# Kernel optimization log

Hardware: AMD Instinct MI355X
Metric: run time of the kernel (lower is better)

Reference implementation:

```python
import jax, jax.numpy as jnp
import numpy as np

B, F, N_SP, VIS_DIM, DIM, HEADS = 2, 16, 784, 512, 512, 8


def setup_inputs() -> dict:
    key = jax.random.key(0)
    k0, k1, k2 = jax.random.split(key, 3)
    x = jax.random.normal(k0, (B, F * N_SP, VIS_DIM), dtype=jnp.float32)
    # QKV: nn.Linear(vis_dim, dim*3, bias=False) -> weight [3*dim, vis_dim]
    Wqkv = jax.random.normal(k1, (3 * DIM, VIS_DIM), dtype=jnp.float32) * 0.02
    # proj: nn.Linear(dim, vis_dim) -> weight [vis_dim, dim], bias [vis_dim]
    Wproj = jax.random.normal(k2, (VIS_DIM, DIM), dtype=jnp.float32) * 0.02
    bproj = jnp.zeros((VIS_DIM,), dtype=jnp.float32)
    return {"x": x, "Wqkv": Wqkv, "Wproj": Wproj, "bproj": bproj,
            "spatial": N_SP, "f": F, "n": N_SP}


def reference(x, Wqkv, Wproj, bproj, spatial, f, n):
    # Factorized (divided space-time) SPATIAL attention:
    # einops_from='b (f n) d', einops_to='(b f) n d' -- attention over n within each frame.
    h = HEADS
    b, seq, _ = x.shape  # seq = f * n
    dim = Wqkv.shape[0] // 3
    hd = dim // h
    scale = hd ** -0.5

    qkv = x @ Wqkv.T                             # [b, f*n, 3*dim]
    q, k, v = jnp.split(qkv, 3, axis=-1)
    rs = lambda t: t.reshape(b, f, n, h, hd)     # b (f n) (h d) -> b f n h d
    q = rs(q) * scale
    k = rs(k)
    v = rs(v)

    # scores over spatial tokens within each (batch, frame, head)
    attn = jax.nn.softmax(jnp.einsum('bfihd,bfjhd->bfhij', q, k), axis=-1)
    out = jnp.einsum('bfhij,bfjhd->bfihd', attn, v)   # [b, f, n, h, hd]
    out = out.reshape(b, seq, dim)               # merge heads + restore (f n)
    return out @ Wproj.T + bproj                 # [b, f*n, vis_dim]
```

## Files before the change

kernel.cpp:

```cpp
#include <hip/hip_runtime.h>
#include <hip/hip_bf16.h>
#include <stdint.h>

using bf16 = __hip_bfloat16;
typedef __bf16 bf16x8 __attribute__((ext_vector_type(8)));
typedef float f32x4  __attribute__((ext_vector_type(4)));
typedef float f32x16 __attribute__((ext_vector_type(16)));

#define NB 2
#define NF 16
#define NSP 784
#define SEQ 12544
#define MROWS 25088
#define QSCALE 0.18033688011112042f

__device__ inline void gload16(const void* g, void* l) {
    __builtin_amdgcn_global_load_lds(
        (const __attribute__((address_space(1))) unsigned int*)g,
        (__attribute__((address_space(3))) unsigned int*)l, 16, 0, 0);
}
__device__ inline ushort f2bu(float x) {
    union { bf16 b; ushort u; } c; c.b = __float2bfloat16(x); return c.u;
}

__global__ __launch_bounds__(256)
void cvt_x_kernel(const float* __restrict__ x, ushort* __restrict__ xb, int n4) {
    int i = blockIdx.x * 256 + threadIdx.x;
    int stride = gridDim.x * 256;
    for (; i < n4; i += stride) {
        float4 v = ((const float4*)x)[i];
        ushort4 u;
        u.x = f2bu(v.x); u.y = f2bu(v.y); u.z = f2bu(v.z); u.w = f2bu(v.w);
        ((ushort4*)xb)[i] = u;
    }
}

__global__ __launch_bounds__(256)
void cvt_w_kernel(const float* __restrict__ wqkv, const float* __restrict__ wproj,
                  ushort* __restrict__ wqkvb, ushort* __restrict__ wpb) {
    int i = blockIdx.x * 256 + threadIdx.x;
    float4 v;
    ushort4 u;
    if (i < 196608) {
        float s = (i < 65536) ? QSCALE : 1.0f;
        v = ((const float4*)wqkv)[i];
        u.x = f2bu(v.x * s); u.y = f2bu(v.y * s);
        u.z = f2bu(v.z * s); u.w = f2bu(v.w * s);
        ((ushort4*)wqkvb)[i] = u;
    } else {
        int j = i - 196608;
        v = ((const float4*)wproj)[j];
        u.x = f2bu(v.x); u.y = f2bu(v.y); u.z = f2bu(v.z); u.w = f2bu(v.w);
        ((ushort4*)wpb)[j] = u;
    }
}

template<int EPI>
__global__ __launch_bounds__(256)
void gemm_mfma(const ushort* __restrict__ A, const ushort* __restrict__ W,
               const float* __restrict__ bias, ushort* __restrict__ outb,
               float* __restrict__ outf, int K, int ldc, int npan)
{
    constexpr int BK  = 64;
    constexpr int SWZ = 7;
    __shared__ ushort smem[16384];

    const int tid = threadIdx.x;
    const int bid = blockIdx.x;
    const int gsz = 4 * npan;
    const int r   = bid % gsz;
    const int m0 = ((bid / gsz) * 4 + (r & 3)) * 128;
    const int n0 = (r >> 2) * 128;
    const int l  = tid & 63;
    const int wv = tid >> 6;
    const int wm = wv >> 1, wn = wv & 1;
    const int lm = l & 15;
    const int koffb = (l >> 4) * 16;
    const int swz = (lm & SWZ) << 4;

    const int rsub = tid >> 3;
    const int cb0  = (tid & 7) * 16;
    const int wofs = (tid >> 6) * 512;

    const size_t ldb = (size_t)K * 2;
    const char* Ab = (const char*)A + (size_t)m0 * ldb;
    const char* Wb = (const char*)W + (size_t)n0 * ldb;

    f32x4 acc[4][4] = {};

    for (int k0 = 0; k0 < K; k0 += BK) {
        if (k0) __syncthreads();
#pragma unroll
        for (int i = 0; i < 4; ++i) {
            int row = i * 32 + rsub;
            int cbs = cb0 ^ ((row & SWZ) << 4);
            size_t roff = (size_t)row * ldb + (size_t)(k0 * 2 + cbs);
            gload16(Ab + roff, smem +        i * 2048 + wofs);
            gload16(Wb + roff, smem + 8192 + i * 2048 + wofs);
        }
        __syncthreads();

#pragma unroll
        for (int ks = 0; ks < 2; ++ks) {
            bf16x8 af[4], wf[4];
            const int cb = ((ks * 64 + koffb) ^ swz) >> 1;
#pragma unroll
            for (int f = 0; f < 4; ++f) {
                int rA = wm * 64 + f * 16 + lm;
                int rW = wn * 64 + f * 16 + lm;
                af[f] = *(const bf16x8*)&smem[rA * BK + cb];
                wf[f] = *(const bf16x8*)&smem[8192 + rW * BK + cb];
            }
            __builtin_amdgcn_s_setprio(1);
#pragma unroll
            for (int fm = 0; fm < 4; ++fm)
#pragma unroll
                for (int fn = 0; fn < 4; ++fn)
                    acc[fm][fn] = __builtin_amdgcn_mfma_f32_16x16x32_bf16(
                        wf[fn], af[fm], acc[fm][fn], 0, 0, 0);
            __builtin_amdgcn_s_setprio(0);
        }
    }

    const int ln4 = (l >> 4) * 4;
    if (EPI == 0) {
#pragma unroll
        for (int fm = 0; fm < 4; ++fm) {
            int m = m0 + wm * 64 + fm * 16 + lm;
            ushort* rowp = outb + (size_t)m * ldc + n0 + wn * 64 + ln4;
#pragma unroll
            for (int fn = 0; fn < 4; ++fn) {
                ushort4 u;
                u.x = f2bu(acc[fm][fn][0]); u.y = f2bu(acc[fm][fn][1]);
                u.z = f2bu(acc[fm][fn][2]); u.w = f2bu(acc[fm][fn][3]);
                *(ushort4*)(rowp + fn * 16) = u;
            }
        }
    } else {
#pragma unroll
        for (int fm = 0; fm < 4; ++fm) {
            int m = m0 + wm * 64 + fm * 16 + lm;
            float* rowp = outf + (size_t)m * ldc + n0 + wn * 64 + ln4;
#pragma unroll
            for (int fn = 0; fn < 4; ++fn) {
                float4 b4 = *(const float4*)&bias[n0 + wn * 64 + fn * 16 + ln4];
                float4 o;
                o.x = acc[fm][fn][0] + b4.x; o.y = acc[fm][fn][1] + b4.y;
                o.z = acc[fm][fn][2] + b4.z; o.w = acc[fm][fn][3] + b4.w;
                *(float4*)(rowp + fn * 16) = o;
            }
        }
    }
}

__global__ __launch_bounds__(256)
void vtrans(const ushort* __restrict__ qkv, ushort* __restrict__ vt)
{
    __shared__ __align__(16) ushort T[256][72];
    const int tid = threadIdx.x;
    const int pr  = blockIdx.x;
    const int c   = blockIdx.y;
    const int hh  = pr & 7, bfi = pr >> 3;
    const ushort* vsrc = qkv + (size_t)bfi * NSP * 1536 + 1024 + hh * 64;
    ushort* dst = vt + (size_t)pr * (64 * NSP);
    const int d = tid & 63, q = tid >> 6;

    const int j0 = c * 256;
    const int nj = (NSP - j0) < 256 ? (NSP - j0) : 256;
    if (tid < nj) {
        const ushort* src = vsrc + (size_t)(j0 + tid) * 1536;
#pragma unroll
        for (int u = 0; u < 8; ++u)
            *(uint4*)&T[tid][u * 8] = *(const uint4*)(src + u * 8);
    }
    __syncthreads();
    if (q * 64 < nj) {
        int cnt = nj - q * 64; if (cnt > 64) cnt = 64;
        union { uint4 u[8]; ushort s[64]; } buf;
#pragma unroll
        for (int jj = 0; jj < 64; ++jj)
            buf.s[jj] = T[q * 64 + jj][d];
        ushort* o = dst + (size_t)d * NSP + j0 + q * 64;
        if (cnt == 64) {
#pragma unroll
            for (int u = 0; u < 8; ++u) *(uint4*)(o + u * 8) = buf.u[u];
        } else {
#pragma unroll
            for (int u = 0; u < 2; ++u) *(uint4*)(o + u * 8) = buf.u[u];
        }
    }
}

__global__ __launch_bounds__(256, 4)
void attn_mfma(const ushort* __restrict__ qkv, const ushort* __restrict__ vt,
               ushort* __restrict__ oh)
{
    __shared__ __align__(16) ushort Ks[2][4096];
    __shared__ __align__(16) ushort Vs[2][4096];
    const int tid = threadIdx.x;
    const int l   = tid & 63;
    const int li  = l & 31;
    const int h5  = l >> 5;
    const int w   = tid >> 6;

    const int bid  = blockIdx.x;
    const int xcd  = bid & 7;
    const int slot = bid >> 3;
    const int pr   = (xcd << 5) + slot / 7;
    const int qt   = slot % 7;
    const int hh   = pr & 7;
    const int bfi  = pr >> 3;
    const size_t rowbase = (size_t)bfi * NSP;
    const int iq = qt * 128 + w * 32 + li;
    const bool qvalid = iq < NSP;
    const int iqc = qvalid ? iq : NSP - 1;

    bf16x8 qf[4];
    {
        const ushort* qrow = qkv + (rowbase + iqc) * 1536 + hh * 64 + h5 * 8;
#pragma unroll
        for (int ks = 0; ks < 4; ++ks)
            qf[ks] = *(const bf16x8*)(qrow + ks * 16);
    }

    const char* kb0   = (const char*)(qkv + rowbase * 1536 + 512 + hh * 64);
    const char* vbase = (const char*)(vt + (size_t)pr * (64 * NSP));

    const int srow = tid >> 3;
    const int sg16 = (tid & 7) * 16;

    float l_run = 0.f;
    f32x16 o0 = {}, o1 = {};

    const int rsw  = (li & 7) << 4;
    const int base0 = li * 128;
    const int base1 = (32 + li) * 128;

#pragma unroll
    for (int i = 0; i < 2; ++i) {
        int row = i * 32 + srow;
        int swz = sg16 ^ ((row & 7) << 4);
        gload16(kb0 + (size_t)row * 3072 + swz, &Ks[0][i * 2048 + tid * 8]);
        gload16(vbase + (size_t)row * 1568 + swz, &Vs[0][i * 2048 + tid * 8]);
    }
    __syncthreads();

    int cur = 0;
    for (int t = 0; t < 13; ++t) {
        const int j0 = t * 64;
        if (t < 12) {
            const int jn = j0 + 64;
#pragma unroll
            for (int i = 0; i < 2; ++i) {
                int row = i * 32 + srow;
                int swz = sg16 ^ ((row & 7) << 4);
                int jr = jn + row; if (jr > NSP - 1) jr = NSP - 1;
                gload16(kb0 + (size_t)jr * 3072 + swz, &Ks[cur ^ 1][i * 2048 + tid * 8]);
                int cb = jn * 2 + swz;
                if (cb + 16 > NSP * 2) cb = jn * 2;
                gload16(vbase + (size_t)row * 1568 + cb, &Vs[cur ^ 1][i * 2048 + tid * 8]);
            }
        }

        const char* KsC = (const char*)&Ks[cur][0];
        const char* VsC = (const char*)&Vs[cur][0];

        f32x16 s0 = {}, s1 = {};
        __builtin_amdgcn_s_setprio(1);
#pragma unroll
        for (int ks = 0; ks < 4; ++ks) {
            int cb = (ks * 32 + h5 * 16) ^ rsw;
            bf16x8 k0 = *(const bf16x8*)(KsC + base0 + cb);
            bf16x8 k1 = *(const bf16x8*)(KsC + base1 + cb);
            s0 = __builtin_amdgcn_mfma_f32_32x32x16_bf16(k0, qf[ks], s0, 0, 0, 0);
            s1 = __builtin_amdgcn_mfma_f32_32x32x16_bf16(k1, qf[ks], s1, 0, 0, 0);
        }
        __builtin_amdgcn_s_setprio(0);

        if (j0 + 64 > NSP) {
#pragma unroll
            for (int r = 0; r < 16; ++r) {
                int jl = (r & 3) + 8 * (r >> 2) + 4 * h5;
                if (j0 + jl >= NSP)      s0[r] = -1e30f;
                if (j0 + 32 + jl >= NSP) s1[r] = -1e30f;
            }
        }

        float p0[16], p1[16];
        float rs = 0.f;
#pragma unroll
        for (int r = 0; r < 16; ++r) { p0[r] = exp2f(s0[r]); rs += p0[r]; }
#pragma unroll
        for (int r = 0; r < 16; ++r) { p1[r] = exp2f(s1[r]); rs += p1[r]; }
        rs += __shfl_xor(rs, 32);
        l_run += rs;

#pragma unroll
        for (int js = 0; js < 4; ++js) {
            const int rb = (js & 1) * 8;
            float e0 = (js < 2) ? p0[rb + 0] : p1[rb + 0];
            float e1 = (js < 2) ? p0[rb + 1] : p1[rb + 1];
            float e2 = (js < 2) ? p0[rb + 2] : p1[rb + 2];
            float e3 = (js < 2) ? p0[rb + 3] : p1[rb + 3];
            float e4 = (js < 2) ? p0[rb + 4] : p1[rb + 4];
            float e5 = (js < 2) ? p0[rb + 5] : p1[rb + 5];
            float e6 = (js < 2) ? p0[rb + 6] : p1[rb + 6];
            float e7 = (js < 2) ? p0[rb + 7] : p1[rb + 7];
            uint A0, A1, B0, B1;
            asm("v_cvt_pk_bf16_f32 %0, %1, %2" : "=v"(A0) : "v"(e0), "v"(e1));
            asm("v_cvt_pk_bf16_f32 %0, %1, %2" : "=v"(A1) : "v"(e2), "v"(e3));
            asm("v_cvt_pk_bf16_f32 %0, %1, %2" : "=v"(B0) : "v"(e4), "v"(e5));
            asm("v_cvt_pk_bf16_f32 %0, %1, %2" : "=v"(B1) : "v"(e6), "v"(e7));
            asm volatile("v_permlane32_swap_b32 %0, %1" : "+v"(A0), "+v"(B0));
            asm volatile("v_permlane32_swap_b32 %0, %1" : "+v"(A1), "+v"(B1));
            union { uint u[4]; bf16x8 v; } pf;
            pf.u[0] = A0; pf.u[1] = A1; pf.u[2] = B0; pf.u[3] = B1;

            int cb = (js * 32 + h5 * 16) ^ rsw;
            bf16x8 v0f = *(const bf16x8*)(VsC + base0 + cb);
            bf16x8 v1f = *(const bf16x8*)(VsC + base1 + cb);
            __builtin_amdgcn_s_setprio(1);
            o0 = __builtin_amdgcn_mfma_f32_32x32x16_bf16(v0f, pf.v, o0, 0, 0, 0);
            o1 = __builtin_amdgcn_mfma_f32_32x32x16_bf16(v1f, pf.v, o1, 0, 0, 0);
            __builtin_amdgcn_s_setprio(0);
        }

        __syncthreads();
        cur ^= 1;
    }

    if (qvalid) {
        float inv = 1.0f / l_run;
        size_t ro = (rowbase + iq) * 512 + hh * 64;
#pragma unroll
        for (int g = 0; g < 4; ++g) {
            int d = g * 8 + h5 * 4;
            ushort4 uh0, uh1;
#pragma unroll
            for (int m = 0; m < 4; ++m) {
                ((ushort*)&uh0)[m] = f2bu(o0[g * 4 + m] * inv);
                ((ushort*)&uh1)[m] = f2bu(o1[g * 4 + m] * inv);
            }
            *(ushort4*)&oh[ro + d]      = uh0;
            *(ushort4*)&oh[ro + 32 + d] = uh1;
        }
    }
}

extern "C" void kernel_launch(void* const* d_in, const int* in_sizes, int n_in,
                              void* d_out, int out_size, void* d_ws, size_t ws_size,
                              hipStream_t stream) {
    const float* x     = (const float*)d_in[0];
    const float* Wqkv  = (const float*)d_in[1];
    const float* Wproj = (const float*)d_in[2];
    const float* bproj = (const float*)d_in[3];
    float* out = (float*)d_out;

    char* ws = (char*)d_ws;
    ushort* xb_ah = (ushort*)(ws);
    ushort* qkvb  = (ushort*)(ws + 25690112);
    ushort* wqkvb = (ushort*)(ws + 102760448);
    ushort* wpb   = (ushort*)(ws + 104333312);

    ushort* vtb = (ushort*)d_out;

    dim3 blk(256);
    cvt_x_kernel<<<2048, blk, 0, stream>>>(x, xb_ah, (MROWS * 512) / 4);
    cvt_w_kernel<<<1024, blk, 0, stream>>>(Wqkv, Wproj, wqkvb, wpb);

    gemm_mfma<0><<<dim3(2352), blk, 0, stream>>>(
        xb_ah, wqkvb, nullptr, qkvb, nullptr, 512, 1536, 12);

    vtrans<<<dim3(256, 4), blk, 0, stream>>>(qkvb, vtb);

    attn_mfma<<<dim3(1792), blk, 0, stream>>>(qkvb, vtb, xb_ah);

    gemm_mfma<1><<<dim3(784), blk, 0, stream>>>(
        xb_ah, wpb, bproj, nullptr, out, 512, 512, 4);
}
```

Measured before the change: 218.7 us.

## Process two 32-query tiles per wave in attention kernel with 128-thread blocks

Each block of the attention kernel drops from four waves to two, and each wave now handles 64 query rows as two 32-row MFMA tiles that share the same K and V fragments read from LDS. This halves LDS fragment reads per unit of MFMA work and doubles the independent MFMAs available to interleave. In exchange it roughly doubles accumulator and score registers per wave, lowers the occupancy hint to 2, and leaves each thread issuing twice as many K/V tile loads.

```diff
diff --git a/kernel.cpp b/kernel.cpp
--- a/kernel.cpp
+++ b/kernel.cpp
@@ -191,17 +191,17 @@
     }
 }
 
-__global__ __launch_bounds__(256, 4)
+__global__ __launch_bounds__(128, 2)
 void attn_mfma(const ushort* __restrict__ qkv, const ushort* __restrict__ vt,
                ushort* __restrict__ oh)
 {
     __shared__ __align__(16) ushort Ks[2][4096];
     __shared__ __align__(16) ushort Vs[2][4096];
     const int tid = threadIdx.x;
+    const int w   = tid >> 6;
     const int l   = tid & 63;
     const int li  = l & 31;
     const int h5  = l >> 5;
-    const int w   = tid >> 6;
 
     const int bid  = blockIdx.x;
     const int xcd  = bid & 7;
@@ -211,37 +211,44 @@
     const int hh   = pr & 7;
     const int bfi  = pr >> 3;
     const size_t rowbase = (size_t)bfi * NSP;
-    const int iq = qt * 128 + w * 32 + li;
-    const bool qvalid = iq < NSP;
-    const int iqc = qvalid ? iq : NSP - 1;
-
-    bf16x8 qf[4];
+
+    const int iqA = qt * 128 + w * 64 + li;
+    const int iqB = iqA + 32;
+    const bool vA = iqA < NSP, vB = iqB < NSP;
+    const int cA = vA ? iqA : NSP - 1;
+    const int cB = vB ? iqB : NSP - 1;
+
+    bf16x8 qa[4], qb[4];
     {
-        const ushort* qrow = qkv + (rowbase + iqc) * 1536 + hh * 64 + h5 * 8;
-#pragma unroll
-        for (int ks = 0; ks < 4; ++ks)
-            qf[ks] = *(const bf16x8*)(qrow + ks * 16);
+        const ushort* ra = qkv + (rowbase + cA) * 1536 + hh * 64 + h5 * 8;
+        const ushort* rb = qkv + (rowbase + cB) * 1536 + hh * 64 + h5 * 8;
+#pragma unroll
+        for (int ks = 0; ks < 4; ++ks) {
+            qa[ks] = *(const bf16x8*)(ra + ks * 16);
+            qb[ks] = *(const bf16x8*)(rb + ks * 16);
+        }
     }
 
     const char* kb0   = (const char*)(qkv + rowbase * 1536 + 512 + hh * 64);
     const char* vbase = (const char*)(vt + (size_t)pr * (64 * NSP));
 
-    const int srow = tid >> 3;
-    const int sg16 = (tid & 7) * 16;
-
-    float l_run = 0.f;
-    f32x16 o0 = {}, o1 = {};
-
-    const int rsw  = (li & 7) << 4;
+    const int srow0 = tid >> 3;
+    const int sg16  = (tid & 7) * 16;
+
+    float lA = 0.f, lB = 0.f;
+    f32x16 oA0 = {}, oA1 = {}, oB0 = {}, oB1 = {};
+    const f32x16 fz = {};
+
+    const int rsw   = (li & 7) << 4;
     const int base0 = li * 128;
     const int base1 = (32 + li) * 128;
 
 #pragma unroll
-    for (int i = 0; i < 2; ++i) {
-        int row = i * 32 + srow;
+    for (int i = 0; i < 4; ++i) {
+        int row = i * 16 + srow0;
         int swz = sg16 ^ ((row & 7) << 4);
-        gload16(kb0 + (size_t)row * 3072 + swz, &Ks[0][i * 2048 + tid * 8]);
-        gload16(vbase + (size_t)row * 1568 + swz, &Vs[0][i * 2048 + tid * 8]);
+        gload16(kb0 + (size_t)row * 3072 + swz, &Ks[0][i * 1024 + tid * 8]);
+        gload16(vbase + (size_t)row * 1568 + swz, &Vs[0][i * 1024 + tid * 8]);
     }
     __syncthreads();
 
@@ -251,29 +258,31 @@
         if (t < 12) {
             const int jn = j0 + 64;
 #pragma unroll
-            for (int i = 0; i < 2; ++i) {
-                int row = i * 32 + srow;
+            for (int i = 0; i < 4; ++i) {
+                int row = i * 16 + srow0;
                 int swz = sg16 ^ ((row & 7) << 4);
                 int jr = jn + row; if (jr > NSP - 1) jr = NSP - 1;
-                gload16(kb0 + (size_t)jr * 3072 + swz, &Ks[cur ^ 1][i * 2048 + tid * 8]);
+                gload16(kb0 + (size_t)jr * 3072 + swz, &Ks[cur ^ 1][i * 1024 + tid * 8]);
                 int cb = jn * 2 + swz;
                 if (cb + 16 > NSP * 2) cb = jn * 2;
-                gload16(vbase + (size_t)row * 1568 + cb, &Vs[cur ^ 1][i * 2048 + tid * 8]);
+                gload16(vbase + (size_t)row * 1568 + cb, &Vs[cur ^ 1][i * 1024 + tid * 8]);
             }
         }
 
         const char* KsC = (const char*)&Ks[cur][0];
         const char* VsC = (const char*)&Vs[cur][0];
 
-        f32x16 s0 = {}, s1 = {};
+        f32x16 sA0 = fz, sA1 = fz, sB0 = fz, sB1 = fz;
         __builtin_amdgcn_s_setprio(1);
 #pragma unroll
         for (int ks = 0; ks < 4; ++ks) {
             int cb = (ks * 32 + h5 * 16) ^ rsw;
             bf16x8 k0 = *(const bf16x8*)(KsC + base0 + cb);
             bf16x8 k1 = *(const bf16x8*)(KsC + base1 + cb);
-            s0 = __builtin_amdgcn_mfma_f32_32x32x16_bf16(k0, qf[ks], s0, 0, 0, 0);
-            s1 = __builtin_amdgcn_mfma_f32_32x32x16_bf16(k1, qf[ks], s1, 0, 0, 0);
+            sA0 = __builtin_amdgcn_mfma_f32_32x32x16_bf16(k0, qa[ks], sA0, 0, 0, 0);
+            sA1 = __builtin_amdgcn_mfma_f32_32x32x16_bf16(k1, qa[ks], sA1, 0, 0, 0);
+            sB0 = __builtin_amdgcn_mfma_f32_32x32x16_bf16(k0, qb[ks], sB0, 0, 0, 0);
+            sB1 = __builtin_amdgcn_mfma_f32_32x32x16_bf16(k1, qb[ks], sB1, 0, 0, 0);
         }
         __builtin_amdgcn_s_setprio(0);
 
@@ -281,47 +290,57 @@
 #pragma unroll
             for (int r = 0; r < 16; ++r) {
                 int jl = (r & 3) + 8 * (r >> 2) + 4 * h5;
-                if (j0 + jl >= NSP)      s0[r] = -1e30f;
-                if (j0 + 32 + jl >= NSP) s1[r] = -1e30f;
-            }
-        }
-
-        float p0[16], p1[16];
-        float rs = 0.f;
-#pragma unroll
-        for (int r = 0; r < 16; ++r) { p0[r] = exp2f(s0[r]); rs += p0[r]; }
-#pragma unroll
-        for (int r = 0; r < 16; ++r) { p1[r] = exp2f(s1[r]); rs += p1[r]; }
-        rs += __shfl_xor(rs, 32);
-        l_run += rs;
+                if (j0 + jl >= NSP)      { sA0[r] = -1e30f; sB0[r] = -1e30f; }
+                if (j0 + 32 + jl >= NSP) { sA1[r] = -1e30f; sB1[r] = -1e30f; }
+            }
+        }
+
+        float ra = 0.f, rb = 0.f;
+#pragma unroll
+        for (int r = 0; r < 16; ++r) {
+            sA0[r] = exp2f(sA0[r]); ra += sA0[r];
+            sA1[r] = exp2f(sA1[r]); ra += sA1[r];
+            sB0[r] = exp2f(sB0[r]); rb += sB0[r];
+            sB1[r] = exp2f(sB1[r]); rb += sB1[r];
+        }
+        ra += __shfl_xor(ra, 32);
+        rb += __shfl_xor(rb, 32);
+        lA += ra; lB += rb;
 
 #pragma unroll
         for (int js = 0; js < 4; ++js) {
-            const int rb = (js & 1) * 8;
-            float e0 = (js < 2) ? p0[rb + 0] : p1[rb + 0];
-            float e1 = (js < 2) ? p0[rb + 1] : p1[rb + 1];
-            float e2 = (js < 2) ? p0[rb + 2] : p1[rb + 2];
-            float e3 = (js < 2) ? p0[rb + 3] : p1[rb + 3];
-            float e4 = (js < 2) ? p0[rb + 4] : p1[rb + 4];
-            float e5 = (js < 2) ? p0[rb + 5] : p1[rb + 5];
-            float e6 = (js < 2) ? p0[rb + 6] : p1[rb + 6];
-            float e7 = (js < 2) ? p0[rb + 7] : p1[rb + 7];
+            const int rb8 = (js & 1) * 8;
             uint A0, A1, B0, B1;
-            asm("v_cvt_pk_bf16_f32 %0, %1, %2" : "=v"(A0) : "v"(e0), "v"(e1));
-            asm("v_cvt_pk_bf16_f32 %0, %1, %2" : "=v"(A1) : "v"(e2), "v"(e3));
-            asm("v_cvt_pk_bf16_f32 %0, %1, %2" : "=v"(B0) : "v"(e4), "v"(e5));
-            asm("v_cvt_pk_bf16_f32 %0, %1, %2" : "=v"(B1) : "v"(e6), "v"(e7));
-            asm volatile("v_permlane32_swap_b32 %0, %1" : "+v"(A0), "+v"(B0));
-            asm volatile("v_permlane32_swap_b32 %0, %1" : "+v"(A1), "+v"(B1));
-            union { uint u[4]; bf16x8 v; } pf;
-            pf.u[0] = A0; pf.u[1] = A1; pf.u[2] = B0; pf.u[3] = B1;
+            union { uint u[4]; bf16x8 v; } pfA, pfB;
+            {
+                const f32x16& s = (js < 2) ? sA0 : sA1;
+                asm("v_cvt_pk_bf16_f32 %0, %1, %2" : "=v"(A0) : "v"(s[rb8+0]), "v"(s[rb8+1]));
+                asm("v_cvt_pk_bf16_f32 %0, %1, %2" : "=v"(A1) : "v"(s[rb8+2]), "v"(s[rb8+3]));
+                asm("v_cvt_pk_bf16_f32 %0, %1, %2" : "=v"(B0) : "v"(s[rb8+4]), "v"(s[rb8+5]));
+                asm("v_cvt_pk_bf16_f32 %0, %1, %2" : "=v"(B1) : "v"(s[rb8+6]), "v"(s[rb8+7]));
+                asm volatile("v_permlane32_swap_b32 %0, %1" : "+v"(A0), "+v"(B0));
+                asm volatile("v_permlane32_swap_b32 %0, %1" : "+v"(A1), "+v"(B1));
+                pfA.u[0] = A0; pfA.u[1] = A1; pfA.u[2] = B0; pfA.u[3] = B1;
+            }
+            {
+                const f32x16& s = (js < 2) ? sB0 : sB1;
+                asm("v_cvt_pk_bf16_f32 %0, %1, %2" : "=v"(A0) : "v"(s[rb8+0]), "v"(s[rb8+1]));
+                asm("v_cvt_pk_bf16_f32 %0, %1, %2" : "=v"(A1) : "v"(s[rb8+2]), "v"(s[rb8+3]));
+                asm("v_cvt_pk_bf16_f32 %0, %1, %2" : "=v"(B0) : "v"(s[rb8+4]), "v"(s[rb8+5]));
+                asm("v_cvt_pk_bf16_f32 %0, %1, %2" : "=v"(B1) : "v"(s[rb8+6]), "v"(s[rb8+7]));
+                asm volatile("v_permlane32_swap_b32 %0, %1" : "+v"(A0), "+v"(B0));
+                asm volatile("v_permlane32_swap_b32 %0, %1" : "+v"(A1), "+v"(B1));
+                pfB.u[0] = A0; pfB.u[1] = A1; pfB.u[2] = B0; pfB.u[3] = B1;
+            }
 
             int cb = (js * 32 + h5 * 16) ^ rsw;
             bf16x8 v0f = *(const bf16x8*)(VsC + base0 + cb);
             bf16x8 v1f = *(const bf16x8*)(VsC + base1 + cb);
             __builtin_amdgcn_s_setprio(1);
-            o0 = __builtin_amdgcn_mfma_f32_32x32x16_bf16(v0f, pf.v, o0, 0, 0, 0);
-            o1 = __builtin_amdgcn_mfma_f32_32x32x16_bf16(v1f, pf.v, o1, 0, 0, 0);
+            oA0 = __builtin_amdgcn_mfma_f32_32x32x16_bf16(v0f, pfA.v, oA0, 0, 0, 0);
+            oA1 = __builtin_amdgcn_mfma_f32_32x32x16_bf16(v1f, pfA.v, oA1, 0, 0, 0);
+            oB0 = __builtin_amdgcn_mfma_f32_32x32x16_bf16(v0f, pfB.v, oB0, 0, 0, 0);
+            oB1 = __builtin_amdgcn_mfma_f32_32x32x16_bf16(v1f, pfB.v, oB1, 0, 0, 0);
             __builtin_amdgcn_s_setprio(0);
         }
 
@@ -329,20 +348,36 @@
         cur ^= 1;
     }
 
-    if (qvalid) {
-        float inv = 1.0f / l_run;
-        size_t ro = (rowbase + iq) * 512 + hh * 64;
+    if (vA) {
+        float inv = 1.0f / lA;
+        size_t ro = (rowbase + iqA) * 512 + hh * 64;
 #pragma unroll
         for (int g = 0; g < 4; ++g) {
             int d = g * 8 + h5 * 4;
-            ushort4 uh0, uh1;
+            ushort4 u0, u1;
 #pragma unroll
             for (int m = 0; m < 4; ++m) {
-                ((ushort*)&uh0)[m] = f2bu(o0[g * 4 + m] * inv);
-                ((ushort*)&uh1)[m] = f2bu(o1[g * 4 + m] * inv);
-            }
-            *(ushort4*)&oh[ro + d]      = uh0;
-            *(ushort4*)&oh[ro + 32 + d] = uh1;
+                ((ushort*)&u0)[m] = f2bu(oA0[g * 4 + m] * inv);
+                ((ushort*)&u1)[m] = f2bu(oA1[g * 4 + m] * inv);
+            }
+            *(ushort4*)&oh[ro + d]      = u0;
+            *(ushort4*)&oh[ro + 32 + d] = u1;
+        }
+    }
+    if (vB) {
+        float inv = 1.0f / lB;
+        size_t ro = (rowbase + iqB) * 512 + hh * 64;
+#pragma unroll
+        for (int g = 0; g < 4; ++g) {
+            int d = g * 8 + h5 * 4;
+            ushort4 u0, u1;
+#pragma unroll
+            for (int m = 0; m < 4; ++m) {
+                ((ushort*)&u0)[m] = f2bu(oB0[g * 4 + m] * inv);
+                ((ushort*)&u1)[m] = f2bu(oB1[g * 4 + m] * inv);
+            }
+            *(ushort4*)&oh[ro + d]      = u0;
+            *(ushort4*)&oh[ro + 32 + d] = u1;
         }
     }
 }
@@ -373,7 +408,7 @@
 
     vtrans<<<dim3(256, 4), blk, 0, stream>>>(qkvb, vtb);
 
-    attn_mfma<<<dim3(1792), blk, 0, stream>>>(qkvb, vtb, xb_ah);
+    attn_mfma<<<dim3(1792), dim3(128), 0, stream>>>(qkvb, vtb, xb_ah);
 
     gemm_mfma<1><<<dim3(784), blk, 0, stream>>>(
         xb_ah, wpb, bproj, nullptr, out, 512, 512, 4);
```

Result: slower. 233.2 us (+6.6%).

## Fuse fp32-to-bf16 conversion of x into QKV GEMM and triple-buffer attention

Applied to the files above, without the earlier changes.

The standalone x conversion kernel is removed. The QKV GEMM now reads fp32 rows of x into registers, converts them to bf16, and writes them into swizzled shared memory, prefetching the next K-tile while the current one is being computed. This avoids one full pass that writes and re-reads x in bf16, but it places register-staged loads and conversion work inside the GEMM loop. The attention kernel also moves from double to triple buffering of K/V tiles, waiting with explicit vmcnt and barriers so loads run two tiles ahead, which lowers the occupancy hint from 4 to 3.

```diff
diff --git a/kernel.cpp b/kernel.cpp
--- a/kernel.cpp
+++ b/kernel.cpp
@@ -21,18 +21,6 @@
 }
 __device__ inline ushort f2bu(float x) {
     union { bf16 b; ushort u; } c; c.b = __float2bfloat16(x); return c.u;
-}
-
-__global__ __launch_bounds__(256)
-void cvt_x_kernel(const float* __restrict__ x, ushort* __restrict__ xb, int n4) {
-    int i = blockIdx.x * 256 + threadIdx.x;
-    int stride = gridDim.x * 256;
-    for (; i < n4; i += stride) {
-        float4 v = ((const float4*)x)[i];
-        ushort4 u;
-        u.x = f2bu(v.x); u.y = f2bu(v.y); u.z = f2bu(v.z); u.w = f2bu(v.w);
-        ((ushort4*)xb)[i] = u;
-    }
 }
 
 __global__ __launch_bounds__(256)
@@ -57,11 +45,11 @@
 
 template<int EPI>
 __global__ __launch_bounds__(256)
-void gemm_mfma(const ushort* __restrict__ A, const ushort* __restrict__ W,
-               const float* __restrict__ bias, ushort* __restrict__ outb,
-               float* __restrict__ outf, int K, int ldc, int npan)
+void gemm_mfma(const float* __restrict__ Af, const ushort* __restrict__ Ab16,
+               const ushort* __restrict__ W, const float* __restrict__ bias,
+               ushort* __restrict__ outb, float* __restrict__ outf,
+               int K, int ldc, int npan)
 {
-    constexpr int BK  = 64;
     constexpr int SWZ = 7;
     __shared__ ushort smem[16384];
 
@@ -83,22 +71,56 @@
     const int wofs = (tid >> 6) * 512;
 
     const size_t ldb = (size_t)K * 2;
-    const char* Ab = (const char*)A + (size_t)m0 * ldb;
     const char* Wb = (const char*)W + (size_t)n0 * ldb;
+    const char* Ab = (EPI == 1) ? (const char*)Ab16 + (size_t)m0 * ldb : nullptr;
+    const float* Afp = (EPI == 0) ? Af + (size_t)m0 * K : nullptr;
+
+    float4 ar0[4], ar1[4];
+    if (EPI == 0) {
+#pragma unroll
+        for (int i = 0; i < 4; ++i) {
+            int row = i * 32 + rsub;
+            const float* src = Afp + (size_t)row * K + (tid & 7) * 8;
+            ar0[i] = *(const float4*)src;
+            ar1[i] = *(const float4*)(src + 4);
+        }
+    }
 
     f32x4 acc[4][4] = {};
 
-    for (int k0 = 0; k0 < K; k0 += BK) {
+    for (int k0 = 0; k0 < K; k0 += 64) {
         if (k0) __syncthreads();
 #pragma unroll
         for (int i = 0; i < 4; ++i) {
             int row = i * 32 + rsub;
             int cbs = cb0 ^ ((row & SWZ) << 4);
             size_t roff = (size_t)row * ldb + (size_t)(k0 * 2 + cbs);
-            gload16(Ab + roff, smem +        i * 2048 + wofs);
             gload16(Wb + roff, smem + 8192 + i * 2048 + wofs);
+            if (EPI == 1) gload16(Ab + roff, smem + i * 2048 + wofs);
+        }
+        if (EPI == 0) {
+#pragma unroll
+            for (int i = 0; i < 4; ++i) {
+                int row = i * 32 + rsub;
+                union { ushort us[8]; bf16x8 v; } pk;
+                pk.us[0] = f2bu(ar0[i].x); pk.us[1] = f2bu(ar0[i].y);
+                pk.us[2] = f2bu(ar0[i].z); pk.us[3] = f2bu(ar0[i].w);
+                pk.us[4] = f2bu(ar1[i].x); pk.us[5] = f2bu(ar1[i].y);
+                pk.us[6] = f2bu(ar1[i].z); pk.us[7] = f2bu(ar1[i].w);
+                int off = row * 64 + ((cb0 ^ ((row & SWZ) << 4)) >> 1);
+                *(bf16x8*)&smem[off] = pk.v;
+            }
         }
         __syncthreads();
+        if (EPI == 0 && k0 + 64 < K) {
+#pragma unroll
+            for (int i = 0; i < 4; ++i) {
+                int row = i * 32 + rsub;
+                const float* src = Afp + (size_t)row * K + (k0 + 64) + (tid & 7) * 8;
+                ar0[i] = *(const float4*)src;
+                ar1[i] = *(const float4*)(src + 4);
+            }
+        }
 
 #pragma unroll
         for (int ks = 0; ks < 2; ++ks) {
@@ -108,8 +130,8 @@
             for (int f = 0; f < 4; ++f) {
                 int rA = wm * 64 + f * 16 + lm;
                 int rW = wn * 64 + f * 16 + lm;
-                af[f] = *(const bf16x8*)&smem[rA * BK + cb];
-                wf[f] = *(const bf16x8*)&smem[8192 + rW * BK + cb];
+                af[f] = *(const bf16x8*)&smem[rA * 64 + cb];
+                wf[f] = *(const bf16x8*)&smem[8192 + rW * 64 + cb];
             }
             __builtin_amdgcn_s_setprio(1);
 #pragma unroll
@@ -191,12 +213,12 @@
     }
 }
 
-__global__ __launch_bounds__(256, 4)
+__global__ __launch_bounds__(256, 3)
 void attn_mfma(const ushort* __restrict__ qkv, const ushort* __restrict__ vt,
                ushort* __restrict__ oh)
 {
-    __shared__ __align__(16) ushort Ks[2][4096];
-    __shared__ __align__(16) ushort Vs[2][4096];
+    __shared__ __align__(16) ushort Ks[3][4096];
+    __shared__ __align__(16) ushort Vs[3][4096];
     const int tid = threadIdx.x;
     const int l   = tid & 63;
     const int li  = l & 31;
@@ -228,42 +250,45 @@
 
     const int srow = tid >> 3;
     const int sg16 = (tid & 7) * 16;
+    const int sswz = sg16 ^ ((srow & 7) << 4);
 
     float l_run = 0.f;
     f32x16 o0 = {}, o1 = {};
 
-    const int rsw  = (li & 7) << 4;
+    const int rsw   = (li & 7) << 4;
     const int base0 = li * 128;
     const int base1 = (32 + li) * 128;
 
 #pragma unroll
-    for (int i = 0; i < 2; ++i) {
-        int row = i * 32 + srow;
-        int swz = sg16 ^ ((row & 7) << 4);
-        gload16(kb0 + (size_t)row * 3072 + swz, &Ks[0][i * 2048 + tid * 8]);
-        gload16(vbase + (size_t)row * 1568 + swz, &Vs[0][i * 2048 + tid * 8]);
-    }
-    __syncthreads();
-
-    int cur = 0;
+    for (int u = 0; u < 2; ++u) {
+#pragma unroll
+        for (int i = 0; i < 2; ++i) {
+            int row = i * 32 + srow;
+            gload16(kb0 + (size_t)(u * 64 + row) * 3072 + sswz, &Ks[u][i * 2048 + tid * 8]);
+            gload16(vbase + (size_t)row * 1568 + u * 128 + sswz, &Vs[u][i * 2048 + tid * 8]);
+        }
+    }
+    asm volatile("s_waitcnt vmcnt(4)" ::: "memory");
+    __builtin_amdgcn_s_barrier();
+
+    int rd = 0;
     for (int t = 0; t < 13; ++t) {
-        const int j0 = t * 64;
-        if (t < 12) {
-            const int jn = j0 + 64;
+        int st = rd + 2; if (st >= 3) st -= 3;
+        if (t < 11) {
+            const int jn = t * 64 + 128;
 #pragma unroll
             for (int i = 0; i < 2; ++i) {
                 int row = i * 32 + srow;
-                int swz = sg16 ^ ((row & 7) << 4);
                 int jr = jn + row; if (jr > NSP - 1) jr = NSP - 1;
-                gload16(kb0 + (size_t)jr * 3072 + swz, &Ks[cur ^ 1][i * 2048 + tid * 8]);
-                int cb = jn * 2 + swz;
+                gload16(kb0 + (size_t)jr * 3072 + sswz, &Ks[st][i * 2048 + tid * 8]);
+                int cb = jn * 2 + sswz;
                 if (cb + 16 > NSP * 2) cb = jn * 2;
-                gload16(vbase + (size_t)row * 1568 + cb, &Vs[cur ^ 1][i * 2048 + tid * 8]);
-            }
-        }
-
-        const char* KsC = (const char*)&Ks[cur][0];
-        const char* VsC = (const char*)&Vs[cur][0];
+                gload16(vbase + (size_t)row * 1568 + cb, &Vs[st][i * 2048 + tid * 8]);
+            }
+        }
+
+        const char* KsC = (const char*)&Ks[rd][0];
+        const char* VsC = (const char*)&Vs[rd][0];
 
         f32x16 s0 = {}, s1 = {};
         __builtin_amdgcn_s_setprio(1);
@@ -277,12 +302,12 @@
         }
         __builtin_amdgcn_s_setprio(0);
 
-        if (j0 + 64 > NSP) {
+        if (t == 12) {
 #pragma unroll
             for (int r = 0; r < 16; ++r) {
                 int jl = (r & 3) + 8 * (r >> 2) + 4 * h5;
-                if (j0 + jl >= NSP)      s0[r] = -1e30f;
-                if (j0 + 32 + jl >= NSP) s1[r] = -1e30f;
+                if (768 + jl >= NSP)      s0[r] = -1e30f;
+                if (768 + 32 + jl >= NSP) s1[r] = -1e30f;
             }
         }
 
@@ -297,15 +322,15 @@
 
 #pragma unroll
         for (int js = 0; js < 4; ++js) {
-            const int rb = (js & 1) * 8;
-            float e0 = (js < 2) ? p0[rb + 0] : p1[rb + 0];
-            float e1 = (js < 2) ? p0[rb + 1] : p1[rb + 1];
-            float e2 = (js < 2) ? p0[rb + 2] : p1[rb + 2];
-            float e3 = (js < 2) ? p0[rb + 3] : p1[rb + 3];
-            float e4 = (js < 2) ? p0[rb + 4] : p1[rb + 4];
-            float e5 = (js < 2) ? p0[rb + 5] : p1[rb + 5];
-            float e6 = (js < 2) ? p0[rb + 6] : p1[rb + 6];
-            float e7 = (js < 2) ? p0[rb + 7] : p1[rb + 7];
+            const int rb8 = (js & 1) * 8;
+            float e0 = (js < 2) ? p0[rb8 + 0] : p1[rb8 + 0];
+            float e1 = (js < 2) ? p0[rb8 + 1] : p1[rb8 + 1];
+            float e2 = (js < 2) ? p0[rb8 + 2] : p1[rb8 + 2];
+            float e3 = (js < 2) ? p0[rb8 + 3] : p1[rb8 + 3];
+            float e4 = (js < 2) ? p0[rb8 + 4] : p1[rb8 + 4];
+            float e5 = (js < 2) ? p0[rb8 + 5] : p1[rb8 + 5];
+            float e6 = (js < 2) ? p0[rb8 + 6] : p1[rb8 + 6];
+            float e7 = (js < 2) ? p0[rb8 + 7] : p1[rb8 + 7];
             uint A0, A1, B0, B1;
             asm("v_cvt_pk_bf16_f32 %0, %1, %2" : "=v"(A0) : "v"(e0), "v"(e1));
             asm("v_cvt_pk_bf16_f32 %0, %1, %2" : "=v"(A1) : "v"(e2), "v"(e3));
@@ -325,8 +350,12 @@
             __builtin_amdgcn_s_setprio(0);
         }
 
-        __syncthreads();
-        cur ^= 1;
+        if (t < 12) {
+            if (t < 11) asm volatile("s_waitcnt vmcnt(4)" ::: "memory");
+            else        asm volatile("s_waitcnt vmcnt(0)" ::: "memory");
+            __builtin_amdgcn_s_barrier();
+        }
+        rd = rd + 1; if (rd >= 3) rd = 0;
     }
 
     if (qvalid) {
@@ -357,7 +386,7 @@
     float* out = (float*)d_out;
 
     char* ws = (char*)d_ws;
-    ushort* xb_ah = (ushort*)(ws);
+    ushort* aout  = (ushort*)(ws);
     ushort* qkvb  = (ushort*)(ws + 25690112);
     ushort* wqkvb = (ushort*)(ws + 102760448);
     ushort* wpb   = (ushort*)(ws + 104333312);
@@ -365,16 +394,15 @@
     ushort* vtb = (ushort*)d_out;
 
     dim3 blk(256);
-    cvt_x_kernel<<<2048, blk, 0, stream>>>(x, xb_ah, (MROWS * 512) / 4);
     cvt_w_kernel<<<1024, blk, 0, stream>>>(Wqkv, Wproj, wqkvb, wpb);
 
     gemm_mfma<0><<<dim3(2352), blk, 0, stream>>>(
-        xb_ah, wqkvb, nullptr, qkvb, nullptr, 512, 1536, 12);
+        x, nullptr, wqkvb, nullptr, qkvb, nullptr, 512, 1536, 12);
 
     vtrans<<<dim3(256, 4), blk, 0, stream>>>(qkvb, vtb);
 
-    attn_mfma<<<dim3(1792), blk, 0, stream>>>(qkvb, vtb, xb_ah);
+    attn_mfma<<<dim3(1792), blk, 0, stream>>>(qkvb, vtb, aout);
 
     gemm_mfma<1><<<dim3(784), blk, 0, stream>>>(
-        xb_ah, wpb, bproj, nullptr, out, 512, 512, 4);
-}
+        nullptr, aout, wpb, bproj, nullptr, out, 512, 512, 4);
+}
```

Result: faster. 211.3 us (-3.4%).
